# Kernel optimization log

Measured on AMD Instinct MI355X. Metric: run time of the kernel, lower is better.

The kernel has to match this reference:

```python
import jax, jax.numpy as jnp
import numpy as np
from jax import lax

H, HD, P, C, HID = 8, 64, 16, 512, 2048
ALIBI_ALPHA, START_I = 1.0, 0
EPS = 1e-5

def setup_inputs():
    key = jax.random.key(0)
    ks = jax.random.split(key, 20)
    s = 0.02
    return {
        "x": jax.random.normal(ks[0], (8, 1024, C), jnp.float32),
        "Wq": jax.random.normal(ks[1], (HD, HD), jnp.float32) * s,
        "Wk": jax.random.normal(ks[2], (HD, HD), jnp.float32) * s,
        "Wv": jax.random.normal(ks[3], (HD, HD), jnp.float32) * s,
        "Wo": jax.random.normal(ks[4], (C, C), jnp.float32) * s,
        "bo": jnp.zeros((C,), jnp.float32),
        "th_pre": jax.random.normal(ks[5], (H, H), jnp.float32) * (1.0 / np.sqrt(H)),
        "th_post": jax.random.normal(ks[6], (H, H), jnp.float32) * (1.0 / np.sqrt(H)),
        "p_keys": jax.random.normal(ks[7], (P, 1, HD), jnp.float32) * s,
        "p_values": jax.random.normal(ks[8], (P, 1, HD), jnp.float32) * s,
        "conv1_w": jax.random.normal(ks[9], (2 * HID, C, 3), jnp.float32) * s,
        "conv1_b": jnp.zeros((2 * HID,), jnp.float32),
        "conv2_w": jax.random.normal(ks[10], (C, HID, 3), jnp.float32) * s,
        "conv2_b": jnp.zeros((C,), jnp.float32),
        "ln1_g": jnp.ones((C,), jnp.float32),
        "ln1_b": jnp.zeros((C,), jnp.float32),
        "ln2_g": jnp.ones((C,), jnp.float32),
        "ln2_b": jnp.zeros((C,), jnp.float32),
    }

def _layernorm(x, g, b):
    mu = jnp.mean(x, axis=-1, keepdims=True)
    var = jnp.mean((x - mu) ** 2, axis=-1, keepdims=True)
    return (x - mu) * lax.rsqrt(var + EPS) * g + b

def _mha(x, Wq, Wk, Wv, Wo, bo, th_pre, th_post, p_keys, p_values):
    N, L, _ = x.shape
    xh = x.reshape(N, L, H, HD)
    q = xh @ Wq.T  # per-head-dim linear, as in torch (applied to last dim)
    k = xh @ Wk.T
    v = xh @ Wv.T
    # persistent memory: [P,1,HD] broadcast over batch and heads
    pk = jnp.broadcast_to(p_keys[None], (N, P, H, HD))
    pv = jnp.broadcast_to(p_values[None], (N, P, H, HD))
    k = jnp.concatenate([k, pk], axis=1)  # (N, L+P, H, HD)
    v = jnp.concatenate([v, pv], axis=1)
    energy = jnp.einsum('nqhd,nkhd->nhqk', q, k)
    # ALiBi: slope_h = 2^(-alpha*(h+1+start_i)), bias = -|q-k|*slope, zero on persistent cols
    slopes = 2.0 ** (-ALIBI_ALPHA * (jnp.arange(1, H + 1, dtype=jnp.float32) + START_I))
    t = jnp.arange(L, dtype=jnp.float32)
    dist = jnp.abs(t[:, None] - t[None, :])  # (L, L)
    bias = -dist[None, :, :] * slopes[:, None, None]  # (H, L, L)
    bias = jnp.pad(bias, ((0, 0), (0, 0), (0, P)))
    energy = energy + bias[None]
    energy = jnp.einsum('gh,nhqk->ngqk', th_pre, energy)  # pre-softmax talking heads (1x1 conv)
    attn = jax.nn.softmax(energy / jnp.sqrt(jnp.float32(C)), axis=-1)
    attn = jnp.einsum('gh,nhqk->ngqk', th_post, attn)  # post-softmax talking heads
    out = jnp.einsum('nhql,nlhd->nqhd', attn, v).reshape(N, L, C)
    return out @ Wo.T + bo

def _ffn(x, conv1_w, conv1_b, conv2_w, conv2_b):
    dn = ('NCH', 'OIH', 'NCH')
    xc = jnp.transpose(x, (0, 2, 1))  # (N, C, L)
    xp = jnp.pad(xc, ((0, 0), (0, 0), (1, 1)))  # same padding, k=3
    h = lax.conv_general_dilated(xp, conv1_w, (1,), 'VALID', dimension_numbers=dn) + conv1_b[None, :, None]
    h1, h2 = jnp.split(h, 2, axis=1)
    h = jax.nn.silu(h1) * h2  # swiglu
    hp = jnp.pad(h, ((0, 0), (0, 0), (1, 1)))
    y = lax.conv_general_dilated(hp, conv2_w, (1,), 'VALID', dimension_numbers=dn) + conv2_b[None, :, None]
    return jnp.transpose(y, (0, 2, 1))

def reference(x, Wq, Wk, Wv, Wo, bo, th_pre, th_post, p_keys, p_values,
              conv1_w, conv1_b, conv2_w, conv2_b, ln1_g, ln1_b, ln2_g, ln2_b):
    a = _mha(x, Wq, Wk, Wv, Wo, bo, th_pre, th_post, p_keys, p_values)
    x1 = _layernorm(a + x, ln1_g, ln1_b)
    f = _ffn(x1, conv1_w, conv1_b, conv2_w, conv2_b)
    return _layernorm(f + x1, ln2_g, ln2_b)
```

## Files before the change

kernel.cpp:

```cpp
#include <hip/hip_runtime.h>
#include <cstddef>
#include <cstdint>

#define NB   8
#define LQ   1024
#define CH   512
#define HHE  8
#define HDD  64
#define PPM  16
#define LP   1040
#define HID  2048

typedef unsigned short ushort_t;
typedef __attribute__((ext_vector_type(8))) short short8;
typedef __attribute__((ext_vector_type(4))) float floatx4;

static const size_t O_QB   = 0;
static const size_t O_KB   = 2097152;
static const size_t O_VB   = 4227072;
static const size_t O_VT   = 6356992;
static const size_t O_AOB  = 8486912;
static const size_t O_AF   = 10584064;
static const size_t O_X1B  = 16777216;
static const size_t O_HPAD = 18878464;
static const size_t O_W1   = 27283456;
static const size_t O_W2   = 30429184;
static const size_t O_WO   = 32002048;

__device__ __forceinline__ ushort_t f2bf(float f) {
  uint32_t u = __float_as_uint(f);
  u += 0x7FFFu + ((u >> 16) & 1u);
  return (ushort_t)(u >> 16);
}
__device__ __forceinline__ float bf2f(ushort_t h) {
  return __uint_as_float(((uint32_t)h) << 16);
}

__device__ __forceinline__ void async16(ushort_t* lds, const ushort_t* g) {
  __builtin_amdgcn_global_load_lds(
      (const __attribute__((address_space(1))) void*)g,
      (__attribute__((address_space(3))) void*)lds, 16, 0, 0);
}

__global__ __launch_bounds__(256) void pack_bf16_kernel(
    const float* __restrict__ src, ushort_t* __restrict__ dst,
    int K, int KD, int icShift)
{
  const int oc = blockIdx.x;
  const int icMask = (1 << icShift) - 1;
  for (int k = threadIdx.x; k < K; k += 256) {
    int ic = k & icMask, dl = k >> icShift;
    dst[(size_t)oc * K + k] = f2bf(src[(size_t)oc * K + ic * KD + dl]);
  }
}

template<int EPI>
__global__ __launch_bounds__(256, 2) void mfma_gemm(
    const ushort_t* __restrict__ Ab, const ushort_t* __restrict__ Bb,
    int K, int BS, int P, int NOUT,
    const float* __restrict__ bias, const float* __restrict__ res,
    float* __restrict__ outf, ushort_t* __restrict__ outh)
{
  __shared__ ushort_t As[128 * 32];
  __shared__ ushort_t Bs[128 * 32];
  const int t = threadIdx.x;
  const int w = t >> 6, l = t & 63;
  const int m0 = blockIdx.x * 128, n0 = blockIdx.y * 128;

  const int kChunk = K / (int)gridDim.z;
  const int kstart = blockIdx.z * kChunk;

  const int sub = l >> 2;
  const int kc8 = (l & 3) * 8;
  const ushort_t* aptr[2];
  const ushort_t* bptr[2];
  #pragma unroll
  for (int c = 0; c < 2; ++c) {
    int arow = m0 + w * 32 + c * 16 + sub;
    aptr[c] = Ab + (size_t)(arow >> 10) * BS + (size_t)(arow & 1023) * P + kc8 + kstart;
    int brow = n0 + w * 32 + c * 16 + sub;
    bptr[c] = Bb + (size_t)brow * K + kc8 + kstart;
  }

  const int wm = w >> 1, wn = w & 1;
  const int lm = l & 15, q = l >> 4;
  floatx4 acc[4][4];
  #pragma unroll
  for (int i = 0; i < 4; ++i)
    #pragma unroll
    for (int j = 0; j < 4; ++j)
      acc[i][j] = (floatx4){0.f, 0.f, 0.f, 0.f};

  const int kIters = kChunk >> 5;
  for (int kt = 0; kt < kIters; ++kt) {
    __syncthreads();
    async16(&As[w * 1024 +   0], aptr[0]);
    async16(&As[w * 1024 + 512], aptr[1]);
    async16(&Bs[w * 1024 +   0], bptr[0]);
    async16(&Bs[w * 1024 + 512], bptr[1]);
    aptr[0] += 32; aptr[1] += 32; bptr[0] += 32; bptr[1] += 32;
    __syncthreads();
    short8 af[4], bf[4];
    #pragma unroll
    for (int i = 0; i < 4; ++i)
      af[i] = *(const short8*)&As[(wm * 64 + i * 16 + lm) * 32 + q * 8];
    #pragma unroll
    for (int i = 0; i < 4; ++i)
      bf[i] = *(const short8*)&Bs[(wn * 64 + i * 16 + lm) * 32 + q * 8];
    #pragma unroll
    for (int i = 0; i < 4; ++i)
      #pragma unroll
      for (int j = 0; j < 4; ++j)
        acc[i][j] = __builtin_amdgcn_mfma_f32_16x16x32_bf16(af[i], bf[j], acc[i][j], 0, 0, 0);
  }

  #pragma unroll
  for (int i = 0; i < 4; ++i) {
    #pragma unroll
    for (int j = 0; j < 4; ++j) {
      const int mbase = m0 + wm * 64 + i * 16 + q * 4;
      const int n = n0 + wn * 64 + j * 16 + lm;
      #pragma unroll
      for (int r = 0; r < 4; ++r) {
        const int m = mbase + r;
        float v = acc[i][j][r];
        if (EPI == 0) {
          outh[(size_t)m * NOUT + n] = f2bf(v);
        } else if (EPI == 1) {
          outf[(size_t)m * NOUT + n] = v + bias[n];
        } else if (EPI == 2) {
          outf[(size_t)m * NOUT + n] = v + bias[n] + res[(size_t)m * NOUT + n];
        } else {
          outf[(size_t)blockIdx.z * 4194304 + (size_t)m * NOUT + n] = v;
        }
      }
    }
  }
}

__global__ __launch_bounds__(256) void ksum_kernel(
    float* __restrict__ pb, const float* __restrict__ bias)
{
  const size_t i = ((size_t)blockIdx.x * 256 + threadIdx.x) * 4;
  float4 a = *(const float4*)&pb[i];
  float4 b = *(const float4*)&pb[i +  4194304];
  float4 c = *(const float4*)&pb[i +  8388608];
  float4 d = *(const float4*)&pb[i + 12582912];
  const int col = (int)(i & 511);
  float4 bi = *(const float4*)&bias[col];
  float4 o;
  o.x = a.x + b.x + c.x + d.x + bi.x;
  o.y = a.y + b.y + c.y + d.y + bi.y;
  o.z = a.z + b.z + c.z + d.z + bi.z;
  o.w = a.w + b.w + c.w + d.w + bi.w;
  *(float4*)&pb[i] = o;
}

__global__ __launch_bounds__(256) void qkv_mfma(
    const float* __restrict__ x,
    const float* __restrict__ Wq, const float* __restrict__ Wk, const float* __restrict__ Wv,
    ushort_t* __restrict__ qo, ushort_t* __restrict__ ko, ushort_t* __restrict__ vo)
{
  __shared__ ushort_t Ws[8 * 512];
  const int mat = blockIdx.y;
  const float* __restrict__ W = (mat == 0) ? Wq : (mat == 1) ? Wk : Wv;
  const int t = threadIdx.x;

  for (int e = t; e < 4096; e += 256) {
    const int oc = e >> 6, ic = e & 63;
    const int nt = oc >> 4, lmm = oc & 15, s = ic >> 5, qd = (ic >> 3) & 3, j = ic & 7;
    Ws[(((nt * 2 + s) * 4 + qd) * 16 + lmm) * 8 + j] = f2bf(W[e]);
  }

  const int w = t >> 6, l = t & 63;
  const int lm = l & 15, quad = l >> 4;
  const int tok0 = blockIdx.x * 64 + w * 16;

  short8 af[16];
  {
    const float* xrow = x + (size_t)(tok0 + lm) * CH + quad * 8;
    #pragma unroll
    for (int h = 0; h < 8; ++h) {
      #pragma unroll
      for (int s = 0; s < 2; ++s) {
        const float4 a = *(const float4*)(xrow + h * 64 + s * 32);
        const float4 b = *(const float4*)(xrow + h * 64 + s * 32 + 4);
        short8 f;
        f[0] = (short)f2bf(a.x); f[1] = (short)f2bf(a.y);
        f[2] = (short)f2bf(a.z); f[3] = (short)f2bf(a.w);
        f[4] = (short)f2bf(b.x); f[5] = (short)f2bf(b.y);
        f[6] = (short)f2bf(b.z); f[7] = (short)f2bf(b.w);
        af[h * 2 + s] = f;
      }
    }
  }
  __syncthreads();

  short8 bfr[8];
  #pragma unroll
  for (int nt = 0; nt < 4; ++nt)
    #pragma unroll
    for (int s = 0; s < 2; ++s)
      bfr[nt * 2 + s] = *(const short8*)&Ws[((nt * 2 + s) * 64 + l) * 8];

  const int n = tok0 >> 10, lpos = tok0 & 1023;
  ushort_t* outp;
  size_t base;
  if (mat == 0) { base = ((size_t)n * LQ + lpos) * CH; outp = qo; }
  else          { base = ((size_t)n * LP + lpos) * CH; outp = (mat == 1) ? ko : vo; }

  #pragma unroll
  for (int h = 0; h < 8; ++h) {
    floatx4 acc[4];
    #pragma unroll
    for (int nt = 0; nt < 4; ++nt) acc[nt] = (floatx4){0.f, 0.f, 0.f, 0.f};
    #pragma unroll
    for (int nt = 0; nt < 4; ++nt)
      #pragma unroll
      for (int s = 0; s < 2; ++s)
        acc[nt] = __builtin_amdgcn_mfma_f32_16x16x32_bf16(
            af[h * 2 + s], bfr[nt * 2 + s], acc[nt], 0, 0, 0);
    #pragma unroll
    for (int nt = 0; nt < 4; ++nt)
      #pragma unroll
      for (int r = 0; r < 4; ++r)
        outp[base + (size_t)(quad * 4 + r) * CH + h * 64 + nt * 16 + lm] =
            f2bf(acc[nt][r]);
  }
}

__global__ __launch_bounds__(256) void persist_kernel(
    const float* __restrict__ pk, const float* __restrict__ pv,
    ushort_t* __restrict__ ko, ushort_t* __restrict__ vo)
{
  const int t = blockIdx.x * 256 + threadIdx.x;
  const int n = t >> 13, p = (t >> 9) & 15, c = t & 511, d = c & 63;
  const size_t o = ((size_t)n * LP + LQ + p) * CH + c;
  ko[o] = f2bf(pk[p * 64 + d]);
  vo[o] = f2bf(pv[p * 64 + d]);
}

__global__ __launch_bounds__(256) void vtrans_kernel(
    const ushort_t* __restrict__ Vb, ushort_t* __restrict__ VT)
{
  __shared__ ushort_t Ls[16 * 520];
  const int n = blockIdx.y, k0 = blockIdx.x * 16;
  const int t = threadIdx.x;
  const int r = t >> 4;
  {
    const ushort_t* src = Vb + ((size_t)(n * LP + k0 + r)) * 512 + (t & 15) * 8;
    ushort_t* dst = &Ls[r * 520 + (t & 15) * 8];
    #pragma unroll
    for (int it = 0; it < 4; ++it)
      *(short8*)(dst + it * 128) = *(const short8*)(src + it * 128);
  }
  __syncthreads();
  #pragma unroll
  for (int rep = 0; rep < 2; ++rep) {
    const int d = t + rep * 256;
    short8 v0, v1;
    #pragma unroll
    for (int j = 0; j < 8; ++j) {
      v0[j] = (short)Ls[j * 520 + d];
      v1[j] = (short)Ls[(8 + j) * 520 + d];
    }
    ushort_t* dst = VT + ((size_t)(n * 512 + d)) * LP + k0;
    *(short8*)(dst)     = v0;
    *(short8*)(dst + 8) = v1;
  }
}

__global__ __launch_bounds__(256, 2) void attn_mfma(
    const ushort_t* __restrict__ Qb, const ushort_t* __restrict__ Kb,
    const ushort_t* __restrict__ VT,
    const float* __restrict__ thpre, const float* __restrict__ thpost,
    ushort_t* __restrict__ aob)
{
  __shared__ __align__(16) char smem[79872];
  ushort_t* Vt  = (ushort_t*)smem;
  float*    Ps  = (float*)(smem + 40960);
  float*    Eb0 = (float*)(smem + 59392);
  float*    Eb1 = (float*)(smem + 69632);
  float*    Ohn = (float*)smem;

  const int n = blockIdx.y, q0 = blockIdx.x * 16;
  const int t = threadIdx.x;
  const int w = t >> 6, l = t & 63;
  const int lm = l & 15, quad = l >> 4;
  const float invs = 0.044194173824159216f;

  short8 qf[4];
  {
    const ushort_t* qrow = Qb + ((size_t)(n * LQ + q0 + lm)) * 512 + (w * 2) * 64 + quad * 8;
    qf[0] = *(const short8*)(qrow);
    qf[1] = *(const short8*)(qrow + 32);
    qf[2] = *(const short8*)(qrow + 64);
    qf[3] = *(const short8*)(qrow + 96);
  }

  float tps[2][8], psl[2], tpo[2][8];
  #pragma unroll
  for (int gg = 0; gg < 2; ++gg) {
    const int g = w * 2 + gg;
    float ps = 0.f;
    #pragma unroll
    for (int h = 0; h < 8; ++h) {
      float tv = thpre[g * 8 + h] * invs;
      tps[gg][h] = tv;
      ps += tv * (1.0f / (float)(2 << h));
      tpo[gg][h] = thpost[g * 8 + h];
    }
    psl[gg] = ps;
  }

  float m_[2][4], z_[2][4];
  #pragma unroll
  for (int gg = 0; gg < 2; ++gg)
    #pragma unroll
    for (int r = 0; r < 4; ++r) { m_[gg][r] = -1e30f; z_[gg][r] = 0.f; }

  floatx4 o_[2][4];
  #pragma unroll
  for (int gg = 0; gg < 2; ++gg)
    #pragma unroll
    for (int ch = 0; ch < 4; ++ch) o_[gg][ch] = (floatx4){0.f, 0.f, 0.f, 0.f};

  const ushort_t* kg  = Kb + ((size_t)(n * LP + lm)) * 512 + (w * 2) * 64 + quad * 8;
  const ushort_t* vgA = VT + ((size_t)(n * 512) + t) * LP;
  const ushort_t* vgB = VT + ((size_t)(n * 512) + t + 256) * LP;

  short8 kfE[4], kfO[4], vX[4], vY[4];

  auto loadKg = [&](short8 (&r)[4], int step) {
    const ushort_t* p = kg + (size_t)step * 8192;
    r[0] = *(const short8*)(p);
    r[1] = *(const short8*)(p + 32);
    r[2] = *(const short8*)(p + 64);
    r[3] = *(const short8*)(p + 96);
  };
  auto loadVg = [&](short8 (&r)[4], int off) {
    r[0] = *(const short8*)(vgA + off); r[1] = *(const short8*)(vgA + off + 8);
    r[2] = *(const short8*)(vgB + off); r[3] = *(const short8*)(vgB + off + 8);
  };
  auto storeV = [&](short8 (&r)[4], int sub) {
    ushort_t* d0 = &Vt[(size_t)t * 40 + sub * 16];
    ushort_t* d1 = &Vt[(size_t)(t + 256) * 40 + sub * 16];
    *(short8*)(d0)     = r[0]; *(short8*)(d0 + 8) = r[1];
    *(short8*)(d1)     = r[2]; *(short8*)(d1 + 8) = r[3];
  };

  auto qktE = [&](short8 (&kf)[4], float* Eb) {
    #pragma unroll
    for (int hh = 0; hh < 2; ++hh) {
      floatx4 e = (floatx4){0.f, 0.f, 0.f, 0.f};
      e = __builtin_amdgcn_mfma_f32_16x16x32_bf16(qf[hh * 2 + 0], kf[hh * 2 + 0], e, 0, 0, 0);
      e = __builtin_amdgcn_mfma_f32_16x16x32_bf16(qf[hh * 2 + 1], kf[hh * 2 + 1], e, 0, 0, 0);
      *(floatx4*)&Eb[(((w * 2 + hh) * 16 + lm)) * 20 + quad * 4] = e;
    }
  };

  auto online2 = [&](int p) {
    float s0[2][4], s1[2][4];
    #pragma unroll
    for (int gg = 0; gg < 2; ++gg)
      #pragma unroll
      for (int r = 0; r < 4; ++r) { s0[gg][r] = 0.f; s1[gg][r] = 0.f; }
    #pragma unroll
    for (int h = 0; h < 8; ++h) {
      const floatx4 a = *(const floatx4*)&Eb0[(h * 16 + lm) * 20 + quad * 4];
      const floatx4 b = *(const floatx4*)&Eb1[(h * 16 + lm) * 20 + quad * 4];
      #pragma unroll
      for (int gg = 0; gg < 2; ++gg) {
        const float tv = tps[gg][h];
        #pragma unroll
        for (int r = 0; r < 4; ++r) {
          s0[gg][r] += tv * a[r];
          s1[gg][r] += tv * b[r];
        }
      }
    }
    const int k0 = 32 * p;
    float pm[2][4];
    #pragma unroll
    for (int r = 0; r < 4; ++r) {
      const float qpos = (float)(q0 + quad * 4 + r);
      const float d0 = fabsf(qpos - (float)(k0 + lm));
      const float d1 = fabsf(qpos - (float)(k0 + 16 + lm));
      #pragma unroll
      for (int gg = 0; gg < 2; ++gg) {
        s0[gg][r] -= d0 * psl[gg];
        s1[gg][r] -= d1 * psl[gg];
        pm[gg][r] = fmaxf(s0[gg][r], s1[gg][r]);
      }
    }
    #pragma unroll
    for (int off = 1; off < 16; off <<= 1)
      #pragma unroll
      for (int gg = 0; gg < 2; ++gg)
        #pragma unroll
        for (int r = 0; r < 4; ++r)
          pm[gg][r] = fmaxf(pm[gg][r], __shfl_xor(pm[gg][r], off));
    float sc[2][4];
    #pragma unroll
    for (int gg = 0; gg < 2; ++gg)
      #pragma unroll
      for (int r = 0; r < 4; ++r) {
        const float mn = fmaxf(m_[gg][r], pm[gg][r]);
        sc[gg][r] = __expf(m_[gg][r] - mn);
        const float p0 = __expf(s0[gg][r] - mn);
        const float p1 = __expf(s1[gg][r] - mn);
        z_[gg][r] = z_[gg][r] * sc[gg][r] + p0 + p1;
        m_[gg][r] = mn;
        float* prow = &Ps[((w * 2 + gg) * 16 + quad * 4 + r) * 36];
        prow[lm] = p0;
        prow[16 + lm] = p1;
      }
    #pragma unroll
    for (int gg = 0; gg < 2; ++gg)
      #pragma unroll
      for (int ch = 0; ch < 4; ++ch)
        #pragma unroll
        for (int r = 0; r < 4; ++r)
          o_[gg][ch][r] *= sc[gg][r];
  };

  auto online1 = [&]() {
    float s0[2][4];
    #pragma unroll
    for (int gg = 0; gg < 2; ++gg)
      #pragma unroll
      for (int r = 0; r < 4; ++r) s0[gg][r] = 0.f;
    #pragma unroll
    for (int h = 0; h < 8; ++h) {
      const floatx4 a = *(const floatx4*)&Eb0[(h * 16 + lm) * 20 + quad * 4];
      #pragma unroll
      for (int gg = 0; gg < 2; ++gg) {
        const float tv = tps[gg][h];
        #pragma unroll
        for (int r = 0; r < 4; ++r) s0[gg][r] += tv * a[r];
      }
    }
    float pm[2][4];
    #pragma unroll
    for (int gg = 0; gg < 2; ++gg)
      #pragma unroll
      for (int r = 0; r < 4; ++r) pm[gg][r] = s0[gg][r];
    #pragma unroll
    for (int off = 1; off < 16; off <<= 1)
      #pragma unroll
      for (int gg = 0; gg < 2; ++gg)
        #pragma unroll
        for (int r = 0; r < 4; ++r)
          pm[gg][r] = fmaxf(pm[gg][r], __shfl_xor(pm[gg][r], off));
    float sc[2][4];
    #pragma unroll
    for (int gg = 0; gg < 2; ++gg)
      #pragma unroll
      for (int r = 0; r < 4; ++r) {
        const float mn = fmaxf(m_[gg][r], pm[gg][r]);
        sc[gg][r] = __expf(m_[gg][r] - mn);
        const float p0 = __expf(s0[gg][r] - mn);
        z_[gg][r] = z_[gg][r] * sc[gg][r] + p0;
        m_[gg][r] = mn;
        float* prow = &Ps[((w * 2 + gg) * 16 + quad * 4 + r) * 36];
        prow[lm] = p0;
        prow[16 + lm] = 0.f;
      }
    #pragma unroll
    for (int gg = 0; gg < 2; ++gg)
      #pragma unroll
      for (int ch = 0; ch < 4; ++ch)
        #pragma unroll
        for (int r = 0; r < 4; ++r)
          o_[gg][ch][r] *= sc[gg][r];
  };

  auto pv = [&]() {
    #pragma unroll
    for (int gg = 0; gg < 2; ++gg) {
      const float4 pa = *(const float4*)&Ps[((w * 2 + gg) * 16 + lm) * 36 + quad * 8];
      const float4 pb = *(const float4*)&Ps[((w * 2 + gg) * 16 + lm) * 36 + quad * 8 + 4];
      short8 pk;
      pk[0] = (short)f2bf(pa.x); pk[1] = (short)f2bf(pa.y);
      pk[2] = (short)f2bf(pa.z); pk[3] = (short)f2bf(pa.w);
      pk[4] = (short)f2bf(pb.x); pk[5] = (short)f2bf(pb.y);
      pk[6] = (short)f2bf(pb.z); pk[7] = (short)f2bf(pb.w);
      #pragma unroll
      for (int ch = 0; ch < 4; ++ch) {
        const int d = (w * 2 + gg) * 64 + ch * 16 + lm;
        const short8 vf = *(const short8*)&Vt[d * 40 + quad * 8];
        o_[gg][ch] = __builtin_amdgcn_mfma_f32_16x16x32_bf16(pk, vf, o_[gg][ch], 0, 0, 0);
      }
    }
  };

  loadKg(kfE, 0);
  loadKg(kfO, 1);
  loadVg(vX, 0);
  loadVg(vY, 16);

  for (int p = 0; p < 32; ++p) {
    qktE(kfE, Eb0);
    qktE(kfO, Eb1);
    loadKg(kfE, 2 * p + 2);
    if (p < 31) loadKg(kfO, 2 * p + 3);
    __syncthreads();
    online2(p);
    storeV(vX, 0);
    storeV(vY, 1);
    loadVg(vX, 32 * (p + 1));
    if (p < 31) loadVg(vY, 32 * (p + 1) + 16);
    __syncthreads();
    pv();
  }
  qktE(kfE, Eb0);
  __syncthreads();
  online1();
  storeV(vX, 0);
  __syncthreads();
  pv();

  #pragma unroll
  for (int off = 1; off < 16; off <<= 1)
    #pragma unroll
    for (int gg = 0; gg < 2; ++gg)
      #pragma unroll
      for (int r = 0; r < 4; ++r)
        z_[gg][r] += __shfl_xor(z_[gg][r], off);
  #pragma unroll
  for (int gg = 0; gg < 2; ++gg)
    #pragma unroll
    for (int r = 0; r < 4; ++r) {
      const float zi = 1.0f / z_[gg][r];
      #pragma unroll
      for (int ch = 0; ch < 4; ++ch) o_[gg][ch][r] *= zi;
    }

  __syncthreads();
  #pragma unroll
  for (int gg = 0; gg < 2; ++gg)
    #pragma unroll
    for (int ch = 0; ch < 4; ++ch)
      #pragma unroll
      for (int r = 0; r < 4; ++r)
        Ohn[(w * 2 + gg) * 1088 + (quad * 4 + r) * 68 + ch * 16 + lm] = o_[gg][ch][r];
  __syncthreads();

  float acc[2][4][4];
  #pragma unroll
  for (int gg = 0; gg < 2; ++gg)
    #pragma unroll
    for (int ch = 0; ch < 4; ++ch)
      #pragma unroll
      for (int r = 0; r < 4; ++r) acc[gg][ch][r] = 0.f;
  #pragma unroll
  for (int h = 0; h < 8; ++h) {
    #pragma unroll
    for (int ch = 0; ch < 4; ++ch)
      #pragma unroll
      for (int r = 0; r < 4; ++r) {
        const float ov = Ohn[h * 1088 + (quad * 4 + r) * 68 + ch * 16 + lm];
        acc[0][ch][r] += tpo[0][h] * ov;
        acc[1][ch][r] += tpo[1][h] * ov;
      }
  }

  #pragma unroll
  for (int gg = 0; gg < 2; ++gg)
    #pragma unroll
    for (int ch = 0; ch < 4; ++ch) {
      const int d = (w * 2 + gg) * 64 + ch * 16 + lm;
      #pragma unroll
      for (int r = 0; r < 4; ++r)
        aob[((size_t)(n * LQ + q0 + quad * 4 + r)) * 512 + d] = f2bf(acc[gg][ch][r]);
    }
}

__global__ __launch_bounds__(256) void swiglu_kernel(
    const ushort_t* __restrict__ hraw, const float* __restrict__ bias,
    ushort_t* __restrict__ hpad)
{
  const int tok = blockIdx.x;
  const int n = tok >> 10, l = tok & 1023;
  const int c = threadIdx.x * 8;
  const size_t src = (size_t)tok * 4096 + c;
  const size_t dst = ((size_t)n * 1026 + l + 1) * 2048 + c;
  const short8 h1v = *(const short8*)&hraw[src];
  const short8 h2v = *(const short8*)&hraw[src + 2048];
  const float4 b1a = *(const float4*)&bias[c];
  const float4 b1b = *(const float4*)&bias[c + 4];
  const float4 b2a = *(const float4*)&bias[2048 + c];
  const float4 b2b = *(const float4*)&bias[2048 + c + 4];
  const float bb1[8] = {b1a.x, b1a.y, b1a.z, b1a.w, b1b.x, b1b.y, b1b.z, b1b.w};
  const float bb2[8] = {b2a.x, b2a.y, b2a.z, b2a.w, b2b.x, b2b.y, b2b.z, b2b.w};
  short8 o;
  #pragma unroll
  for (int j = 0; j < 8; ++j) {
    const float h1 = bf2f((ushort_t)h1v[j]) + bb1[j];
    const float h2 = bf2f((ushort_t)h2v[j]) + bb2[j];
    const float s = h1 / (1.f + __expf(-h1));
    o[j] = (short)f2bf(s * h2);
  }
  *(short8*)&hpad[dst] = o;
}

__global__ __launch_bounds__(256) void zero_pads_kernel(
    ushort_t* __restrict__ x1b, ushort_t* __restrict__ hpad)
{
  const int b = blockIdx.x;
  const int n = b >> 1, side = b & 1;
  const size_t r = (size_t)n * 1026 + side * 1025;
  ushort2 z; z.x = 0; z.y = 0;
  *(ushort2*)&x1b[r * 512 + threadIdx.x * 2] = z;
  #pragma unroll
  for (int i = 0; i < 4; ++i)
    *(ushort2*)&hpad[r * 2048 + (threadIdx.x + 256 * i) * 2] = z;
}

__global__ __launch_bounds__(256) void ln_kernel(
    const float* __restrict__ in, const float* __restrict__ res,
    const float* __restrict__ g, const float* __restrict__ b,
    float* __restrict__ outp, ushort_t* __restrict__ bfout)
{
  const int w = threadIdx.x >> 6, lane = threadIdx.x & 63;
  const int tok = blockIdx.x * 4 + w;
  const size_t base = (size_t)tok * CH;
  float4 v0 = *(const float4*)&in[base + (lane << 2)];
  float4 v1 = *(const float4*)&in[base + 256 + (lane << 2)];
  if (res != nullptr) {
    float4 r0 = *(const float4*)&res[base + (lane << 2)];
    float4 r1 = *(const float4*)&res[base + 256 + (lane << 2)];
    v0.x += r0.x; v0.y += r0.y; v0.z += r0.z; v0.w += r0.w;
    v1.x += r1.x; v1.y += r1.y; v1.z += r1.z; v1.w += r1.w;
  }
  float s = v0.x + v0.y + v0.z + v0.w + v1.x + v1.y + v1.z + v1.w;
  #pragma unroll
  for (int off = 32; off > 0; off >>= 1) s += __shfl_xor(s, off);
  const float mu = s * (1.f / 512.f);
  float d0 = v0.x - mu, d1 = v0.y - mu, d2 = v0.z - mu, d3 = v0.w - mu;
  float d4 = v1.x - mu, d5 = v1.y - mu, d6 = v1.z - mu, d7 = v1.w - mu;
  float vs = d0*d0 + d1*d1 + d2*d2 + d3*d3 + d4*d4 + d5*d5 + d6*d6 + d7*d7;
  #pragma unroll
  for (int off = 32; off > 0; off >>= 1) vs += __shfl_xor(vs, off);
  const float r = rsqrtf(vs * (1.f / 512.f) + 1e-5f);
  float4 ga = *(const float4*)&g[(lane << 2)];
  float4 gb = *(const float4*)&g[256 + (lane << 2)];
  float4 ba = *(const float4*)&b[(lane << 2)];
  float4 bb = *(const float4*)&b[256 + (lane << 2)];
  float4 o0, o1;
  o0.x = d0 * r * ga.x + ba.x; o0.y = d1 * r * ga.y + ba.y;
  o0.z = d2 * r * ga.z + ba.z; o0.w = d3 * r * ga.w + ba.w;
  o1.x = d4 * r * gb.x + bb.x; o1.y = d5 * r * gb.y + bb.y;
  o1.z = d6 * r * gb.z + bb.z; o1.w = d7 * r * gb.w + bb.w;
  *(float4*)&outp[base + (lane << 2)] = o0;
  *(float4*)&outp[base + 256 + (lane << 2)] = o1;
  if (bfout != nullptr) {
    const int n = tok >> 10, ll = tok & 1023;
    const size_t bb2 = ((size_t)n * 1026 + ll + 1) * 512;
    ushort4 u0 = make_ushort4(f2bf(o0.x), f2bf(o0.y), f2bf(o0.z), f2bf(o0.w));
    ushort4 u1 = make_ushort4(f2bf(o1.x), f2bf(o1.y), f2bf(o1.z), f2bf(o1.w));
    *(ushort4*)&bfout[bb2 + (lane << 2)] = u0;
    *(ushort4*)&bfout[bb2 + 256 + (lane << 2)] = u1;
  }
}

extern "C" void kernel_launch(void* const* d_in, const int* in_sizes, int n_in,
                              void* d_out, int out_size, void* d_ws, size_t ws_size,
                              hipStream_t stream)
{
  (void)in_sizes; (void)n_in; (void)out_size; (void)ws_size;
  const float* x      = (const float*)d_in[0];
  const float* Wq     = (const float*)d_in[1];
  const float* Wk     = (const float*)d_in[2];
  const float* Wv     = (const float*)d_in[3];
  const float* Wo     = (const float*)d_in[4];
  const float* bo     = (const float*)d_in[5];
  const float* th_pre = (const float*)d_in[6];
  const float* th_post= (const float*)d_in[7];
  const float* p_keys = (const float*)d_in[8];
  const float* p_vals = (const float*)d_in[9];
  const float* c1w    = (const float*)d_in[10];
  const float* c1b    = (const float*)d_in[11];
  const float* c2w    = (const float*)d_in[12];
  const float* c2b    = (const float*)d_in[13];
  const float* ln1g   = (const float*)d_in[14];
  const float* ln1b   = (const float*)d_in[15];
  const float* ln2g   = (const float*)d_in[16];
  const float* ln2b   = (const float*)d_in[17];

  float* ws  = (float*)d_ws;
  float* out = (float*)d_out;

  ushort_t* Qb   = (ushort_t*)(ws + O_QB);
  ushort_t* Kb   = (ushort_t*)(ws + O_KB);
  ushort_t* Vb   = (ushort_t*)(ws + O_VB);
  ushort_t* VT   = (ushort_t*)(ws + O_VT);
  ushort_t* aob  = (ushort_t*)(ws + O_AOB);
  float*    abf  = ws + O_AF;
  ushort_t* x1b  = (ushort_t*)(ws + O_X1B);
  ushort_t* hpad = (ushort_t*)(ws + O_HPAD);
  ushort_t* hraw = (ushort_t*)ws;
  float*    pk4  = ws;
  ushort_t* w1p  = (ushort_t*)(ws + O_W1);
  ushort_t* w2p  = (ushort_t*)(ws + O_W2);
  ushort_t* wop  = (ushort_t*)(ws + O_WO);

  pack_bf16_kernel<<<4096, 256, 0, stream>>>(c1w, w1p, 1536, 3, 9);
  pack_bf16_kernel<<<512,  256, 0, stream>>>(c2w, w2p, 6144, 3, 11);
  pack_bf16_kernel<<<512,  256, 0, stream>>>(Wo,  wop, 512,  1, 9);

  qkv_mfma<<<dim3(128, 3), 256, 0, stream>>>(x, Wq, Wk, Wv, Qb, Kb, Vb);
  persist_kernel<<<256, 256, 0, stream>>>(p_keys, p_vals, Kb, Vb);
  vtrans_kernel<<<dim3(65, 8), 256, 0, stream>>>(Vb, VT);

  attn_mfma<<<dim3(64, 8), 256, 0, stream>>>(Qb, Kb, VT, th_pre, th_post, aob);

  mfma_gemm<2><<<dim3(64, 4), 256, 0, stream>>>(
      aob, wop, 512, 1024 * 512, 512, 512, bo, x, abf, nullptr);

  ln_kernel<<<2048, 256, 0, stream>>>(abf, nullptr, ln1g, ln1b, out, x1b);
  zero_pads_kernel<<<16, 256, 0, stream>>>(x1b, hpad);

  mfma_gemm<0><<<dim3(64, 32), 256, 0, stream>>>(
      x1b, w1p, 1536, 1026 * 512, 512, 4096, nullptr, nullptr, nullptr, hraw);

  swiglu_kernel<<<8192, 256, 0, stream>>>(hraw, c1b, hpad);

  mfma_gemm<3><<<dim3(64, 4, 4), 256, 0, stream>>>(
      hpad, w2p, 6144, 1026 * 2048, 2048, 512, nullptr, nullptr, pk4, nullptr);
  ksum_kernel<<<4096, 256, 0, stream>>>(pk4, c2b);

  ln_kernel<<<2048, 256, 0, stream>>>(pk4, out, ln2g, ln2b, out, nullptr);
}
```

Baseline: 530.9 us.

## Software-pipeline attention loop with bf16 LDS score buffers and warp-local V tiles

```diff
diff --git a/kernel.cpp b/kernel.cpp
--- a/kernel.cpp
+++ b/kernel.cpp
@@ -276,11 +276,10 @@
     const float* __restrict__ thpre, const float* __restrict__ thpost,
     ushort_t* __restrict__ aob)
 {
-  __shared__ __align__(16) char smem[79872];
+  __shared__ __align__(16) char smem[71680];
   ushort_t* Vt  = (ushort_t*)smem;
-  float*    Ps  = (float*)(smem + 40960);
-  float*    Eb0 = (float*)(smem + 59392);
-  float*    Eb1 = (float*)(smem + 69632);
+  ushort_t* Psb = (ushort_t*)(smem + 40960);
+  ushort_t* Eb  = (ushort_t*)(smem + 51200);
   float*    Ohn = (float*)smem;
 
   const int n = blockIdx.y, q0 = blockIdx.x * 16;
@@ -326,8 +325,8 @@
     for (int ch = 0; ch < 4; ++ch) o_[gg][ch] = (floatx4){0.f, 0.f, 0.f, 0.f};
 
   const ushort_t* kg  = Kb + ((size_t)(n * LP + lm)) * 512 + (w * 2) * 64 + quad * 8;
-  const ushort_t* vgA = VT + ((size_t)(n * 512) + t) * LP;
-  const ushort_t* vgB = VT + ((size_t)(n * 512) + t + 256) * LP;
+  const ushort_t* vgA = VT + ((size_t)(n * 512) + w * 128 + l) * LP;
+  const ushort_t* vgB = VT + ((size_t)(n * 512) + w * 128 + 64 + l) * LP;
 
   short8 kfE[4], kfO[4], vX[4], vY[4];
 
@@ -343,23 +342,27 @@
     r[2] = *(const short8*)(vgB + off); r[3] = *(const short8*)(vgB + off + 8);
   };
   auto storeV = [&](short8 (&r)[4], int sub) {
-    ushort_t* d0 = &Vt[(size_t)t * 40 + sub * 16];
-    ushort_t* d1 = &Vt[(size_t)(t + 256) * 40 + sub * 16];
+    ushort_t* d0 = &Vt[(size_t)(w * 128 + l) * 40 + sub * 16];
+    ushort_t* d1 = &Vt[(size_t)(w * 128 + 64 + l) * 40 + sub * 16];
     *(short8*)(d0)     = r[0]; *(short8*)(d0 + 8) = r[1];
     *(short8*)(d1)     = r[2]; *(short8*)(d1 + 8) = r[3];
   };
 
-  auto qktE = [&](short8 (&kf)[4], float* Eb) {
+  auto qktE = [&](short8 (&kf)[4], ushort_t* E) {
     #pragma unroll
     for (int hh = 0; hh < 2; ++hh) {
       floatx4 e = (floatx4){0.f, 0.f, 0.f, 0.f};
       e = __builtin_amdgcn_mfma_f32_16x16x32_bf16(qf[hh * 2 + 0], kf[hh * 2 + 0], e, 0, 0, 0);
       e = __builtin_amdgcn_mfma_f32_16x16x32_bf16(qf[hh * 2 + 1], kf[hh * 2 + 1], e, 0, 0, 0);
-      *(floatx4*)&Eb[(((w * 2 + hh) * 16 + lm)) * 20 + quad * 4] = e;
+      ushort4 u;
+      u.x = f2bf(e[0]); u.y = f2bf(e[1]); u.z = f2bf(e[2]); u.w = f2bf(e[3]);
+      *(ushort4*)&E[(((w * 2 + hh) * 16 + lm)) * 20 + quad * 4] = u;
     }
   };
 
   auto online2 = [&](int p) {
+    const ushort_t* Ea = Eb + ((2 * p) & 3) * 2560;
+    const ushort_t* Ec = Eb + ((2 * p + 1) & 3) * 2560;
     float s0[2][4], s1[2][4];
     #pragma unroll
     for (int gg = 0; gg < 2; ++gg)
@@ -367,15 +370,17 @@
       for (int r = 0; r < 4; ++r) { s0[gg][r] = 0.f; s1[gg][r] = 0.f; }
     #pragma unroll
     for (int h = 0; h < 8; ++h) {
-      const floatx4 a = *(const floatx4*)&Eb0[(h * 16 + lm) * 20 + quad * 4];
-      const floatx4 b = *(const floatx4*)&Eb1[(h * 16 + lm) * 20 + quad * 4];
+      const ushort4 ua = *(const ushort4*)&Ea[(h * 16 + lm) * 20 + quad * 4];
+      const ushort4 ub = *(const ushort4*)&Ec[(h * 16 + lm) * 20 + quad * 4];
+      const float a_[4] = {bf2f(ua.x), bf2f(ua.y), bf2f(ua.z), bf2f(ua.w)};
+      const float b_[4] = {bf2f(ub.x), bf2f(ub.y), bf2f(ub.z), bf2f(ub.w)};
       #pragma unroll
       for (int gg = 0; gg < 2; ++gg) {
         const float tv = tps[gg][h];
         #pragma unroll
         for (int r = 0; r < 4; ++r) {
-          s0[gg][r] += tv * a[r];
-          s1[gg][r] += tv * b[r];
+          s0[gg][r] += tv * a_[r];
+          s1[gg][r] += tv * b_[r];
         }
       }
     }
@@ -411,9 +416,9 @@
         const float p1 = __expf(s1[gg][r] - mn);
         z_[gg][r] = z_[gg][r] * sc[gg][r] + p0 + p1;
         m_[gg][r] = mn;
-        float* prow = &Ps[((w * 2 + gg) * 16 + quad * 4 + r) * 36];
-        prow[lm] = p0;
-        prow[16 + lm] = p1;
+        ushort_t* prow = &Psb[((w * 2 + gg) * 16 + quad * 4 + r) * 40];
+        prow[lm] = f2bf(p0);
+        prow[16 + lm] = f2bf(p1);
       }
     #pragma unroll
     for (int gg = 0; gg < 2; ++gg)
@@ -425,6 +430,7 @@
   };
 
   auto online1 = [&]() {
+    const ushort_t* Ea = Eb;
     float s0[2][4];
     #pragma unroll
     for (int gg = 0; gg < 2; ++gg)
@@ -432,12 +438,13 @@
       for (int r = 0; r < 4; ++r) s0[gg][r] = 0.f;
     #pragma unroll
     for (int h = 0; h < 8; ++h) {
-      const floatx4 a = *(const floatx4*)&Eb0[(h * 16 + lm) * 20 + quad * 4];
+      const ushort4 ua = *(const ushort4*)&Ea[(h * 16 + lm) * 20 + quad * 4];
+      const float a_[4] = {bf2f(ua.x), bf2f(ua.y), bf2f(ua.z), bf2f(ua.w)};
       #pragma unroll
       for (int gg = 0; gg < 2; ++gg) {
         const float tv = tps[gg][h];
         #pragma unroll
-        for (int r = 0; r < 4; ++r) s0[gg][r] += tv * a[r];
+        for (int r = 0; r < 4; ++r) s0[gg][r] += tv * a_[r];
       }
     }
     float pm[2][4];
@@ -462,9 +469,9 @@
         const float p0 = __expf(s0[gg][r] - mn);
         z_[gg][r] = z_[gg][r] * sc[gg][r] + p0;
         m_[gg][r] = mn;
-        float* prow = &Ps[((w * 2 + gg) * 16 + quad * 4 + r) * 36];
-        prow[lm] = p0;
-        prow[16 + lm] = 0.f;
+        ushort_t* prow = &Psb[((w * 2 + gg) * 16 + quad * 4 + r) * 40];
+        prow[lm] = f2bf(p0);
+        prow[16 + lm] = 0;
       }
     #pragma unroll
     for (int gg = 0; gg < 2; ++gg)
@@ -478,13 +485,7 @@
   auto pv = [&]() {
     #pragma unroll
     for (int gg = 0; gg < 2; ++gg) {
-      const float4 pa = *(const float4*)&Ps[((w * 2 + gg) * 16 + lm) * 36 + quad * 8];
-      const float4 pb = *(const float4*)&Ps[((w * 2 + gg) * 16 + lm) * 36 + quad * 8 + 4];
-      short8 pk;
-      pk[0] = (short)f2bf(pa.x); pk[1] = (short)f2bf(pa.y);
-      pk[2] = (short)f2bf(pa.z); pk[3] = (short)f2bf(pa.w);
-      pk[4] = (short)f2bf(pb.x); pk[5] = (short)f2bf(pb.y);
-      pk[6] = (short)f2bf(pb.z); pk[7] = (short)f2bf(pb.w);
+      const short8 pk = *(const short8*)&Psb[((w * 2 + gg) * 16 + lm) * 40 + quad * 8];
       #pragma unroll
       for (int ch = 0; ch < 4; ++ch) {
         const int d = (w * 2 + gg) * 64 + ch * 16 + lm;
@@ -498,26 +499,30 @@
   loadKg(kfO, 1);
   loadVg(vX, 0);
   loadVg(vY, 16);
+  qktE(kfE, Eb + 0 * 2560);
+  qktE(kfO, Eb + 1 * 2560);
+  loadKg(kfE, 2);
+  loadKg(kfO, 3);
+  __syncthreads();
 
   for (int p = 0; p < 32; ++p) {
-    qktE(kfE, Eb0);
-    qktE(kfO, Eb1);
-    loadKg(kfE, 2 * p + 2);
-    if (p < 31) loadKg(kfO, 2 * p + 3);
-    __syncthreads();
+    __builtin_amdgcn_s_setprio(1);
+    if (p > 0) pv();
+    qktE(kfE, Eb + ((2 * p + 2) & 3) * 2560);
+    if (p < 31) qktE(kfO, Eb + ((2 * p + 3) & 3) * 2560);
+    __builtin_amdgcn_s_setprio(0);
     online2(p);
     storeV(vX, 0);
     storeV(vY, 1);
+    if (p < 30)       { loadKg(kfE, 2 * p + 4); loadKg(kfO, 2 * p + 5); }
+    else if (p == 30) { loadKg(kfE, 64); }
     loadVg(vX, 32 * (p + 1));
     if (p < 31) loadVg(vY, 32 * (p + 1) + 16);
     __syncthreads();
-    pv();
-  }
-  qktE(kfE, Eb0);
-  __syncthreads();
+  }
+  pv();
   online1();
   storeV(vX, 0);
-  __syncthreads();
   pv();
 
   #pragma unroll
```

Measured after the change: 526.3 us. Within noise of the previous version (-0.9%).
